# Kernel tuning notes

Hardware: AMD Instinct MI355X
Metric: run time of the kernel (lower is better)

Reference implementation:

```python
import jax, jax.numpy as jnp
import numpy as np

B, S, D, H = 4, 2048, 1024, 16
HD = D // H

def setup_inputs() -> dict:
    key = jax.random.key(0)
    k1, k2, k3, k4, k5 = jax.random.split(key, 5)
    sc = 1.0 / np.sqrt(D)
    return {
        "x": jax.random.normal(k1, (B, S, D), dtype=jnp.float32),
        "w_qkv": jax.random.normal(k2, (D, 3 * D), dtype=jnp.float32) * sc,
        "b_qkv": jnp.zeros((3 * D,), dtype=jnp.float32),
        "w_proj": jax.random.normal(k3, (D, D), dtype=jnp.float32) * sc,
        "b_proj": jnp.zeros((D,), dtype=jnp.float32),
    }

def reference(x, w_qkv, b_qkv, w_proj, b_proj):
    bsz, seq_len, dim = x.shape
    qkv = x @ w_qkv + b_qkv                      # [B,S,3D]
    q, k, v = jnp.split(qkv, 3, axis=2)
    q = q.reshape(bsz, seq_len, H, HD).transpose(0, 2, 1, 3)  # [B,H,S,hd]
    k = k.reshape(bsz, seq_len, H, HD).transpose(0, 2, 1, 3)
    v = v.reshape(bsz, seq_len, H, HD).transpose(0, 2, 1, 3)
    att = jnp.einsum('bhqd,bhkd->bhqk', q, k) * (1.0 / np.sqrt(HD))
    causal = jnp.tril(jnp.ones((seq_len, seq_len), dtype=bool))
    att = jnp.where(causal[None, None], att, -jnp.inf)
    att = jax.nn.softmax(att, axis=-1)
    y = jnp.einsum('bhqk,bhkd->bhqd', att, v)
    y = y.transpose(0, 2, 1, 3).reshape(bsz, seq_len, dim)
    return y @ w_proj + b_proj
```

## Files before the change

kernel.cpp:

```cpp
#include <hip/hip_runtime.h>
#include <cstdint>
#include <cstddef>

typedef float  f32x4  __attribute__((ext_vector_type(4)));
typedef __bf16 bf16x8 __attribute__((ext_vector_type(8)));
typedef __bf16 bf16x4 __attribute__((ext_vector_type(4)));

#define DEVI static __device__ __forceinline__

DEVI f32x4 mfma_bf16(bf16x8 a, bf16x8 b, f32x4 c) {
  return __builtin_amdgcn_mfma_f32_16x16x32_bf16(a, b, c, 0, 0, 0);
}

DEVI void gload_lds16(const void* g, void* l) {
  __builtin_amdgcn_global_load_lds(
      (const __attribute__((address_space(1))) void*)g,
      (__attribute__((address_space(3))) void*)l, 16, 0, 0);
}

__global__ void k_cast_bf16(const float* __restrict__ src, __bf16* __restrict__ dst, int n4) {
  int i = blockIdx.x * blockDim.x + threadIdx.x;
  if (i < n4) {
    float4 v = reinterpret_cast<const float4*>(src)[i];
    bf16x4 r;
    r.x = (__bf16)v.x; r.y = (__bf16)v.y; r.z = (__bf16)v.z; r.w = (__bf16)v.w;
    reinterpret_cast<bf16x4*>(dst)[i] = r;
  }
}

__global__ void k_transpose_cast(const float* __restrict__ src, __bf16* __restrict__ dst,
                                 int R, int C) {
  __shared__ __bf16 tile[64][65];
  const int tx = threadIdx.x & 63, ty = threadIdx.x >> 6;
  const int r0 = blockIdx.y * 64, c0 = blockIdx.x * 64;
#pragma unroll
  for (int i = 0; i < 16; ++i) {
    int r = ty * 16 + i;
    tile[r][tx] = (__bf16)src[(size_t)(r0 + r) * C + c0 + tx];
  }
  __syncthreads();
#pragma unroll
  for (int i = 0; i < 16; ++i) {
    int c = ty * 16 + i;
    dst[(size_t)(c0 + c) * R + r0 + tx] = tile[tx][c];
  }
}

__global__ void k_transpose_v(const __bf16* __restrict__ qkv, __bf16* __restrict__ VT) {
  __shared__ __bf16 tile[64][65];
  const int tx = threadIdx.x & 63, ty = threadIdx.x >> 6;
  const int bh = blockIdx.y;
  const int b = bh >> 4, h = bh & 15;
  const int s0 = blockIdx.x * 64;
  const __bf16* src = qkv + (size_t)(b * 2048) * 3072 + 2048 + h * 64;
#pragma unroll
  for (int i = 0; i < 16; ++i) {
    int s = ty * 16 + i;
    tile[s][tx] = src[(size_t)(s0 + s) * 3072 + tx];
  }
  __syncthreads();
  __bf16* dst = VT + (size_t)bh * 64 * 2048;
#pragma unroll
  for (int i = 0; i < 16; ++i) {
    int d = ty * 16 + i;
    dst[(size_t)d * 2048 + s0 + tx] = tile[tx][d];
  }
}

template <int MODE>
__global__ __launch_bounds__(256, 2) void k_gemm_bt(
    const __bf16* __restrict__ A, const __bf16* __restrict__ Bt,
    const float* __restrict__ bias, void* __restrict__ Cv,
    int M, int N, int K, int nbx) {
  __shared__ __bf16 As[128 * 64];
  __shared__ __bf16 Bs[128 * 64];
  const int t = threadIdx.x;
  const int w = t >> 6, lane = t & 63;
  const int l15 = lane & 15, lg = lane >> 4;
  const int m0 = (blockIdx.x / nbx) * 128;
  const int n0 = (blockIdx.x % nbx) * 128;
  const int wr = w >> 1, wc = w & 1;
  const int lrow = lane >> 3, lslot = lane & 7;

  f32x4 acc[4][4] = {};

  const int nK = K >> 6;
  for (int kt = 0; kt < nK; ++kt) {
    const __bf16* Ab = A + (size_t)m0 * K + kt * 64;
    const __bf16* Bb = Bt + (size_t)n0 * K + kt * 64;
#pragma unroll
    for (int c = 0; c < 4; ++c) {
      int seg = w * 4 + c;
      int row = seg * 8 + lrow;
      int cb = (lslot ^ (row & 7)) << 4;
      gload_lds16((const char*)(Ab + (size_t)row * K) + cb, (char*)As + seg * 1024);
      gload_lds16((const char*)(Bb + (size_t)row * K) + cb, (char*)Bs + seg * 1024);
    }
    __syncthreads();
#pragma unroll
    for (int ks = 0; ks < 2; ++ks) {
      bf16x8 af[4], bfr[4];
      const int cb = ks * 64 + (lg << 4);
#pragma unroll
      for (int m = 0; m < 4; ++m) {
        int row = wr * 64 + m * 16 + l15;
        af[m] = *(const bf16x8*)((const char*)As + row * 128 + (cb ^ ((row & 7) << 4)));
      }
#pragma unroll
      for (int n = 0; n < 4; ++n) {
        int row = wc * 64 + n * 16 + l15;
        bfr[n] = *(const bf16x8*)((const char*)Bs + row * 128 + (cb ^ ((row & 7) << 4)));
      }
#pragma unroll
      for (int m = 0; m < 4; ++m)
#pragma unroll
        for (int n = 0; n < 4; ++n)
          acc[m][n] = mfma_bf16(af[m], bfr[n], acc[m][n]);
    }
    __syncthreads();
  }

#pragma unroll
  for (int n = 0; n < 4; ++n) {
    const int gcol = n0 + wc * 64 + n * 16 + l15;
    const float bv = bias ? bias[gcol] : 0.0f;
#pragma unroll
    for (int m = 0; m < 4; ++m) {
      const int grow = m0 + wr * 64 + m * 16 + (lg << 2);
#pragma unroll
      for (int r = 0; r < 4; ++r) {
        float v = acc[m][n][r] + bv;
        if (MODE == 0)
          ((__bf16*)Cv)[(size_t)(grow + r) * N + gcol] = (__bf16)v;
        else
          ((float*)Cv)[(size_t)(grow + r) * N + gcol] = v;
      }
    }
  }
}

__global__ __launch_bounds__(256, 2) void k_attn(
    const __bf16* __restrict__ qkv,
    const __bf16* __restrict__ VT,
    __bf16* __restrict__ Y) {
  __shared__ __bf16 kbuf[2][64 * 64];
  __shared__ __bf16 vbuf[2][64 * 64];
  __shared__ __bf16 p_lds[4][1024];
  const int t = threadIdx.x, w = t >> 6, lane = t & 63;
  const int l15 = lane & 15, lg = lane >> 4;
  const int bid = blockIdx.x;
  const int qt = 31 - (bid >> 6);
  const int bh = bid & 63;
  const int b = bh >> 4, h = bh & 15;
  const int q0 = qt * 64;
  const int nkv = qt + 1;
  const float SCL = 0.125f * 1.44269504f;

  const size_t qrow = (size_t)(b * 2048 + q0 + w * 16 + l15);
  const bf16x8 qf0 = *(const bf16x8*)(qkv + qrow * 3072 + h * 64 + lg * 8);
  const bf16x8 qf1 = *(const bf16x8*)(qkv + qrow * 3072 + h * 64 + 32 + lg * 8);

  const __bf16* kg = qkv + (size_t)(b * 2048) * 3072 + 1024 + h * 64;
  const __bf16* vg = VT + (size_t)bh * 64 * 2048;

  const int srow = lane >> 3, sslot = lane & 7;
  auto stage = [&](int bi, int kvi) {
#pragma unroll
    for (int i = 0; i < 2; ++i) {
      int row = i * 32 + w * 8 + srow;
      int sb = (sslot ^ (row & 7)) << 4;
      gload_lds16((const char*)(kg + (size_t)(kvi * 64 + row) * 3072) + sb,
                  (char*)kbuf[bi] + i * 4096 + w * 1024);
      gload_lds16((const char*)(vg + (size_t)row * 2048 + kvi * 64) + sb,
                  (char*)vbuf[bi] + i * 4096 + w * 1024);
    }
  };

  f32x4 o[4] = {};
  float mr = -1e30f, lr = 0.0f;
  __bf16* pl = &p_lds[w][0];

  stage(0, 0);
  asm volatile("s_waitcnt vmcnt(0)" ::: "memory");
  __syncthreads();

  for (int kv = 0; kv < nkv; ++kv) {
    if (kv + 1 < nkv) stage((kv + 1) & 1, kv + 1);
    const char* kb = (const char*)kbuf[kv & 1];
    const char* vb = (const char*)vbuf[kv & 1];

    f32x4 s[4] = {};
    __builtin_amdgcn_s_setprio(1);
#pragma unroll
    for (int nb = 0; nb < 4; ++nb) {
      int row = nb * 16 + l15;
      int sw = (row & 7) << 4;
      bf16x8 k0 = *(const bf16x8*)(kb + row * 128 + ((lg * 16) ^ sw));
      bf16x8 k1 = *(const bf16x8*)(kb + row * 128 + ((64 + lg * 16) ^ sw));
      s[nb] = mfma_bf16(k0, qf0, s[nb]);
      s[nb] = mfma_bf16(k1, qf1, s[nb]);
    }
    __builtin_amdgcn_s_setprio(0);

    if (kv == qt) {
      const int qg = q0 + w * 16 + l15;
#pragma unroll
      for (int nb = 0; nb < 4; ++nb)
#pragma unroll
        for (int r = 0; r < 4; ++r)
          if (kv * 64 + nb * 16 + lg * 4 + r > qg) s[nb][r] = -1e30f;
    }

    float pm = -3e38f;
#pragma unroll
    for (int nb = 0; nb < 4; ++nb)
      pm = fmaxf(pm, fmaxf(fmaxf(s[nb][0], s[nb][1]), fmaxf(s[nb][2], s[nb][3])));
    pm = fmaxf(pm, __shfl_xor(pm, 16));
    pm = fmaxf(pm, __shfl_xor(pm, 32));
    pm *= SCL;

    if (!__all(pm <= mr + 8.0f)) {
      float nm = fmaxf(mr, pm);
      float alpha = __builtin_amdgcn_exp2f(mr - nm);
      lr *= alpha;
      mr = nm;
#pragma unroll
      for (int r = 0; r < 4; ++r) {
        float aO = __shfl(alpha, lg * 4 + r);
        o[0][r] *= aO; o[1][r] *= aO; o[2][r] *= aO; o[3][r] *= aO;
      }
    }

    float ps = 0.0f;
    bf16x4 pk[4];
#pragma unroll
    for (int nb = 0; nb < 4; ++nb) {
      f32x4 pe;
#pragma unroll
      for (int r = 0; r < 4; ++r)
        pe[r] = __builtin_amdgcn_exp2f(fmaf(s[nb][r], SCL, -mr));
      ps += (pe[0] + pe[1]) + (pe[2] + pe[3]);
      pk[nb][0] = (__bf16)pe[0]; pk[nb][1] = (__bf16)pe[1];
      pk[nb][2] = (__bf16)pe[2]; pk[nb][3] = (__bf16)pe[3];
    }
    ps += __shfl_xor(ps, 16);
    ps += __shfl_xor(ps, 32);
    lr += ps;

    {
      const int rowb = l15 * 128;
      const int sw = (l15 & 7) << 4;
#pragma unroll
      for (int nb = 0; nb < 4; ++nb) {
        int cb = (nb * 32 + lg * 8) ^ sw;
        *(bf16x4*)((char*)pl + rowb + cb) = pk[nb];
      }
    }
    asm volatile("s_waitcnt lgkmcnt(0)" ::: "memory");
    bf16x8 pf0, pf1;
    {
      const int rowb = l15 * 128;
      const int sw = (l15 & 7) << 4;
      pf0 = *(const bf16x8*)((const char*)pl + rowb + ((lg << 4) ^ sw));
      pf1 = *(const bf16x8*)((const char*)pl + rowb + ((64 + (lg << 4)) ^ sw));
    }
    __builtin_amdgcn_s_setprio(1);
#pragma unroll
    for (int nb = 0; nb < 4; ++nb) {
      int row = nb * 16 + l15;
      int sw = (row & 7) << 4;
      bf16x8 v0 = *(const bf16x8*)(vb + row * 128 + ((lg * 16) ^ sw));
      bf16x8 v1 = *(const bf16x8*)(vb + row * 128 + ((64 + lg * 16) ^ sw));
      o[nb] = mfma_bf16(pf0, v0, o[nb]);
      o[nb] = mfma_bf16(pf1, v1, o[nb]);
    }
    __builtin_amdgcn_s_setprio(0);
    asm volatile("s_waitcnt vmcnt(0)" ::: "memory");
    __syncthreads();
  }

  float lO[4];
#pragma unroll
  for (int r = 0; r < 4; ++r) lO[r] = __shfl(lr, lg * 4 + r);
#pragma unroll
  for (int nb = 0; nb < 4; ++nb)
#pragma unroll
    for (int r = 0; r < 4; ++r) {
      float v = o[nb][r] / lO[r];
      size_t row = (size_t)(b * 2048 + q0 + w * 16 + lg * 4 + r);
      Y[row * 1024 + h * 64 + nb * 16 + l15] = (__bf16)v;
    }
}

extern "C" void kernel_launch(void* const* d_in, const int* in_sizes, int n_in,
                              void* d_out, int out_size, void* d_ws, size_t ws_size,
                              hipStream_t stream) {
  const float* x      = (const float*)d_in[0];
  const float* w_qkv  = (const float*)d_in[1];
  const float* b_qkv  = (const float*)d_in[2];
  const float* w_proj = (const float*)d_in[3];
  const float* b_proj = (const float*)d_in[4];
  float* out = (float*)d_out;

  char* ws = (char*)d_ws;
  const size_t MB = 1024 * 1024;
  __bf16* xb     = (__bf16*)(ws);
  __bf16* wqkvT  = (__bf16*)(ws + 16 * MB);
  __bf16* wprojT = (__bf16*)(ws + 22 * MB);
  __bf16* qkv    = (__bf16*)(ws + 24 * MB);
  __bf16* VT     = (__bf16*)(ws + 72 * MB);
  __bf16* Y      = (__bf16*)(ws + 88 * MB);

  k_cast_bf16<<<8192, 256, 0, stream>>>(x, xb, 8192 * 1024 / 4);
  k_transpose_cast<<<dim3(48, 16), 256, 0, stream>>>(w_qkv, wqkvT, 1024, 3072);
  k_transpose_cast<<<dim3(16, 16), 256, 0, stream>>>(w_proj, wprojT, 1024, 1024);
  k_gemm_bt<0><<<dim3(64 * 24), 256, 0, stream>>>(xb, wqkvT, b_qkv, qkv, 8192, 3072, 1024, 24);
  k_transpose_v<<<dim3(32, 64), 256, 0, stream>>>(qkv, VT);
  k_attn<<<dim3(2048), 256, 0, stream>>>(qkv, VT, Y);
  k_gemm_bt<1><<<dim3(64 * 8), 256, 0, stream>>>(Y, wprojT, b_proj, out, 8192, 1024, 1024, 8);
}
```

Measured before the change: 188.0 us.

## Triple-buffer GEMM with 128x256 tiles, 512 threads and XCD-aware block remap

Replaces the single-buffered GEMM with a three-stage LDS ring that prefetches two K-tiles ahead and waits with explicit vmcnt counts and raw barriers. This is meant to hide global-load latency behind the MFMA work. The tile grows to 128x256 on 8 waves, block IDs are remapped across XCDs for better L2 locality, and s_setprio is raised around the MFMA bursts. In exchange, LDS use rises to about 144KB per block, which likely allows only one block per CU despite the launch bound of 2. The hand-written vmcnt counts also risk stage hazards.

```diff
diff --git a/kernel.cpp b/kernel.cpp
--- a/kernel.cpp
+++ b/kernel.cpp
@@ -68,56 +68,86 @@
 }
 
 template <int MODE>
-__global__ __launch_bounds__(256, 2) void k_gemm_bt(
+__global__ __launch_bounds__(512, 2) void k_gemm3(
     const __bf16* __restrict__ A, const __bf16* __restrict__ Bt,
     const float* __restrict__ bias, void* __restrict__ Cv,
     int M, int N, int K, int nbx) {
-  __shared__ __bf16 As[128 * 64];
-  __shared__ __bf16 Bs[128 * 64];
+  __shared__ __bf16 Ab[3][128 * 64];
+  __shared__ __bf16 Bb[3][256 * 64];
   const int t = threadIdx.x;
   const int w = t >> 6, lane = t & 63;
   const int l15 = lane & 15, lg = lane >> 4;
-  const int m0 = (blockIdx.x / nbx) * 128;
-  const int n0 = (blockIdx.x % nbx) * 128;
-  const int wr = w >> 1, wc = w & 1;
-  const int lrow = lane >> 3, lslot = lane & 7;
+  const int wr = w & 1, wc = w >> 1;
+
+  const int nwg = gridDim.x;
+  const int wgid = (blockIdx.x & 7) * (nwg >> 3) + (blockIdx.x >> 3);
+  const int m0 = (wgid / nbx) * 128;
+  const int n0 = (wgid % nbx) * 256;
+
+  const int tid8 = t >> 3, slot = t & 7;
+  const int swb = (slot ^ (tid8 & 7)) << 4;
+  const char* pA0 = (const char*)(A + (size_t)(m0 + tid8) * K) + swb;
+  const char* pB0 = (const char*)(Bt + (size_t)(n0 + tid8) * K) + swb;
+  const size_t ROWS64 = (size_t)64 * K * 2;
+
+  auto stage = [&](int buf, int kt) {
+    const size_t ko = (size_t)kt * 128;
+#pragma unroll
+    for (int i = 0; i < 2; ++i)
+      gload_lds16(pA0 + ko + i * ROWS64, (char*)Ab[buf] + i * 8192 + w * 1024);
+#pragma unroll
+    for (int i = 0; i < 4; ++i)
+      gload_lds16(pB0 + ko + i * ROWS64, (char*)Bb[buf] + i * 8192 + w * 1024);
+  };
+
+  int offA[4], offB[4];
+#pragma unroll
+  for (int m = 0; m < 4; ++m) {
+    int row = wr * 64 + m * 16 + l15;
+    offA[m] = row * 128 + ((lg * 16) ^ ((row & 7) << 4));
+  }
+#pragma unroll
+  for (int n = 0; n < 4; ++n) {
+    int row = wc * 64 + n * 16 + l15;
+    offB[n] = row * 128 + ((lg * 16) ^ ((row & 7) << 4));
+  }
 
   f32x4 acc[4][4] = {};
-
   const int nK = K >> 6;
+
+  stage(0, 0);
+  stage(1, 1);
+  asm volatile("s_waitcnt vmcnt(6)" ::: "memory");
+  __builtin_amdgcn_s_barrier();
+
   for (int kt = 0; kt < nK; ++kt) {
-    const __bf16* Ab = A + (size_t)m0 * K + kt * 64;
-    const __bf16* Bb = Bt + (size_t)n0 * K + kt * 64;
-#pragma unroll
-    for (int c = 0; c < 4; ++c) {
-      int seg = w * 4 + c;
-      int row = seg * 8 + lrow;
-      int cb = (lslot ^ (row & 7)) << 4;
-      gload_lds16((const char*)(Ab + (size_t)row * K) + cb, (char*)As + seg * 1024);
-      gload_lds16((const char*)(Bb + (size_t)row * K) + cb, (char*)Bs + seg * 1024);
-    }
-    __syncthreads();
+    const int buf = kt % 3;
+    const bool pf = (kt + 2) < nK;
+    if (pf) stage((kt + 2) % 3, kt + 2);
+    const char* ab = (const char*)Ab[buf];
+    const char* bb = (const char*)Bb[buf];
 #pragma unroll
     for (int ks = 0; ks < 2; ++ks) {
+      const int kx = ks << 6;
       bf16x8 af[4], bfr[4];
-      const int cb = ks * 64 + (lg << 4);
-#pragma unroll
-      for (int m = 0; m < 4; ++m) {
-        int row = wr * 64 + m * 16 + l15;
-        af[m] = *(const bf16x8*)((const char*)As + row * 128 + (cb ^ ((row & 7) << 4)));
-      }
-#pragma unroll
-      for (int n = 0; n < 4; ++n) {
-        int row = wc * 64 + n * 16 + l15;
-        bfr[n] = *(const bf16x8*)((const char*)Bs + row * 128 + (cb ^ ((row & 7) << 4)));
-      }
+#pragma unroll
+      for (int m = 0; m < 4; ++m) af[m] = *(const bf16x8*)(ab + (offA[m] ^ kx));
+#pragma unroll
+      for (int n = 0; n < 4; ++n) bfr[n] = *(const bf16x8*)(bb + (offB[n] ^ kx));
+      __builtin_amdgcn_s_setprio(1);
 #pragma unroll
       for (int m = 0; m < 4; ++m)
 #pragma unroll
         for (int n = 0; n < 4; ++n)
           acc[m][n] = mfma_bf16(af[m], bfr[n], acc[m][n]);
-    }
-    __syncthreads();
+      __builtin_amdgcn_s_setprio(0);
+    }
+    if (pf) {
+      asm volatile("s_waitcnt vmcnt(6)" ::: "memory");
+    } else {
+      asm volatile("s_waitcnt vmcnt(0)" ::: "memory");
+    }
+    __builtin_amdgcn_s_barrier();
   }
 
 #pragma unroll
@@ -314,8 +344,8 @@
   k_cast_bf16<<<8192, 256, 0, stream>>>(x, xb, 8192 * 1024 / 4);
   k_transpose_cast<<<dim3(48, 16), 256, 0, stream>>>(w_qkv, wqkvT, 1024, 3072);
   k_transpose_cast<<<dim3(16, 16), 256, 0, stream>>>(w_proj, wprojT, 1024, 1024);
-  k_gemm_bt<0><<<dim3(64 * 24), 256, 0, stream>>>(xb, wqkvT, b_qkv, qkv, 8192, 3072, 1024, 24);
+  k_gemm3<0><<<dim3(64 * 12), 512, 0, stream>>>(xb, wqkvT, b_qkv, qkv, 8192, 3072, 1024, 12);
   k_transpose_v<<<dim3(32, 64), 256, 0, stream>>>(qkv, VT);
   k_attn<<<dim3(2048), 256, 0, stream>>>(qkv, VT, Y);
-  k_gemm_bt<1><<<dim3(64 * 8), 256, 0, stream>>>(Y, wprojT, b_proj, out, 8192, 1024, 1024, 8);
-}
+  k_gemm3<1><<<dim3(64 * 4), 512, 0, stream>>>(Y, wprojT, b_proj, out, 8192, 1024, 1024, 4);
+}
```

Result: slower. 198.4 us (+5.5%).
